# Kernel optimization log

Measured on AMD Instinct MI355X. Metric: run time of the kernel, lower is better.

The kernel has to match this reference:

```python
import jax, jax.numpy as jnp
import numpy as np

WINDOW = 8


def _one_hot_kernel(window):
    # kernel[i//w, i%w, 0, i] = 1 -> extracts each pixel of a w*w sliding window
    k = np.zeros((window, window, 1, window * window), dtype=np.float32)
    for i in range(window * window):
        k[i // window, i % window, 0, i] = 1.0
    return jnp.asarray(k)


def setup_inputs() -> dict:
    key = jax.random.key(0)
    inputs = jax.random.normal(key, (8, 512, 512, 1), dtype=jnp.float32)
    kernel = _one_hot_kernel(WINDOW)  # (8, 8, 1, 64), HWIO
    return {"inputs": inputs, "kernel": kernel}


def reference(inputs, kernel):
    # Faithful translation of keras.backend.conv2d(inputs, kernel):
    # VALID padding, stride 1, NHWC data / HWIO kernel.
    # Mathematically this is im2col/unfold: out[b,h,w,i] = inputs[b, h+i//W, w+i%W, 0].
    y = jax.lax.conv_general_dilated(
        inputs, kernel,
        window_strides=(1, 1),
        padding="VALID",
        dimension_numbers=("NHWC", "HWIO", "NHWC"),
    )
    return y  # (B, H-7, W-7, 64)
```

## Files before the change

### kernel.cpp

```cpp
#include <hip/hip_runtime.h>


#define BATCH   8
#define W_IN    512
#define HW_OUT  505
#define ROW4    (HW_OUT * 16)
#define LDS_STRIDE 516

typedef float f32x4 __attribute__((ext_vector_type(4)));

__global__ __launch_bounds__(256) void unfold_lds_kernel(
    const float* __restrict__ in, float* __restrict__ out)
{
    __shared__ float smem[8 * LDS_STRIDE];

    int bh = blockIdx.x;
    int b  = bh / HW_OUT;
    int h  = bh - b * HW_OUT;

    const float* __restrict__ row_base = in + (b * W_IN + h) * W_IN;
    f32x4* __restrict__ out4 = reinterpret_cast<f32x4*>(out) + (size_t)bh * ROW4;

    for (int t = threadIdx.x; t < 8 * 128; t += 256) {
        int r = t >> 7;
        int q = t & 127;
        f32x4 v = *reinterpret_cast<const f32x4*>(row_base + (r << 9) + (q << 2));
        *reinterpret_cast<f32x4*>(&smem[r * LDS_STRIDE + (q << 2)]) = v;
    }
    __syncthreads();

    for (int t = threadIdx.x; t < ROW4; t += 256) {
        int i4 = t & 15;
        int w  = t >> 4;
        int r  = i4 >> 1;
        int c  = (i4 & 1) << 2;

        const float* __restrict__ s = &smem[r * LDS_STRIDE + w + c];
        f32x4 v;
        v.x = s[0];
        v.y = s[1];
        v.z = s[2];
        v.w = s[3];
        out4[t] = v;
    }
}

extern "C" void kernel_launch(void* const* d_in, const int* in_sizes, int n_in,
                              void* d_out, int out_size, void* d_ws, size_t ws_size,
                              hipStream_t stream)
{
    const float* in  = (const float*)d_in[0];
    float*       out = (float*)d_out;

    const int grid = BATCH * HW_OUT;
    unfold_lds_kernel<<<grid, 256, 0, stream>>>(in, out);
}
```

Before: 104.2 us.

## Split output rows into 32-column tiles with persistent grid-stride blocks

```diff
diff --git a/kernel.cpp b/kernel.cpp
--- a/kernel.cpp
+++ b/kernel.cpp
@@ -5,43 +5,56 @@
 #define W_IN    512
 #define HW_OUT  505
 #define ROW4    (HW_OUT * 16)
-#define LDS_STRIDE 516
+#define SEGS    16
+#define SEG4    512
+#define TILES   (BATCH * HW_OUT * SEGS)
+#define SW      40
 
 typedef float f32x4 __attribute__((ext_vector_type(4)));
 
-__global__ __launch_bounds__(256) void unfold_lds_kernel(
+__global__ __launch_bounds__(256) void unfold_tile_kernel(
     const float* __restrict__ in, float* __restrict__ out)
 {
-    __shared__ float smem[8 * LDS_STRIDE];
+    __shared__ float sm[8 * SW];
 
-    int bh = blockIdx.x;
-    int b  = bh / HW_OUT;
-    int h  = bh - b * HW_OUT;
+    f32x4* __restrict__ out4 = reinterpret_cast<f32x4*>(out);
 
-    const float* __restrict__ row_base = in + (b * W_IN + h) * W_IN;
-    f32x4* __restrict__ out4 = reinterpret_cast<f32x4*>(out) + (size_t)bh * ROW4;
+    for (int tile = blockIdx.x; tile < TILES; tile += gridDim.x) {
+        int bh  = tile >> 4;
+        int seg = tile & 15;
+        int b   = bh / HW_OUT;
+        int h   = bh - b * HW_OUT;
+        int w0  = seg << 5;
 
-    for (int t = threadIdx.x; t < 8 * 128; t += 256) {
-        int r = t >> 7;
-        int q = t & 127;
-        f32x4 v = *reinterpret_cast<const f32x4*>(row_base + (r << 9) + (q << 2));
-        *reinterpret_cast<f32x4*>(&smem[r * LDS_STRIDE + (q << 2)]) = v;
-    }
-    __syncthreads();
+        const float* __restrict__ row_base = in + (b * W_IN + h) * W_IN;
 
-    for (int t = threadIdx.x; t < ROW4; t += 256) {
-        int i4 = t & 15;
-        int w  = t >> 4;
-        int r  = i4 >> 1;
-        int c  = (i4 & 1) << 2;
+        for (int s = threadIdx.x; s < 8 * SW; s += 256) {
+            int r   = s / SW;
+            int j   = s - r * SW;
+            int col = w0 + j;
+            sm[s] = (col < W_IN) ? row_base[(r << 9) + col] : 0.0f;
+        }
+        __syncthreads();
 
-        const float* __restrict__ s = &smem[r * LDS_STRIDE + w + c];
-        f32x4 v;
-        v.x = s[0];
-        v.y = s[1];
-        v.z = s[2];
-        v.w = s[3];
-        out4[t] = v;
+        int n4 = SEG4;
+        if (seg == SEGS - 1) n4 = ROW4 - (SEGS - 1) * SEG4;
+        f32x4* __restrict__ o = out4 + (size_t)bh * ROW4 + seg * SEG4;
+
+        for (int t = threadIdx.x; t < n4; t += 256) {
+            int i4 = t & 15;
+            int p  = t >> 4;
+            int r  = i4 >> 1;
+            int c  = (i4 & 1) << 2;
+
+            const float* __restrict__ s = &sm[r * SW + p + c];
+            f32x4 v;
+            v.x = s[0];
+            v.y = s[1];
+            v.z = s[2];
+            v.w = s[3];
+            o[t] = v;
+        }
+        __syncthreads();
     }
 }
 
@@ -52,6 +65,6 @@
     const float* in  = (const float*)d_in[0];
     float*       out = (float*)d_out;
 
-    const int grid = BATCH * HW_OUT;
-    unfold_lds_kernel<<<grid, 256, 0, stream>>>(in, out);
+    const int grid = 2048;
+    unfold_tile_kernel<<<grid, 256, 0, stream>>>(in, out);
 }
```

Result: slower. 114.0 us (+9.4%).
